# Performance work log

Hardware: AMD Instinct MI355X
Metric: run time of the kernel (lower is better)

Reference implementation:

```python
import jax, jax.numpy as jnp
import numpy as np

N_SRC = 50000   # source nodes in the block
N_DST = 50000   # destination nodes
E = 800000      # edges (avg in-degree 16, every dst has >=1 edge)
D = 256         # hidden_dim
V = 50000       # vocab_size
C = 104         # n_classes (POJ-104)


def setup_inputs() -> dict:
    key = jax.random.key(0)
    k1, k2, k3, k4, k5, k6 = jax.random.split(key, 6)
    token_id = jax.random.randint(k1, (N_SRC,), 0, V, dtype=jnp.int32)
    src_idx = jax.random.randint(k2, (E,), 0, N_SRC, dtype=jnp.int32)
    # every dst node gets at least one in-edge (DGL raises on 0-in-degree),
    # remaining edges land on random dst nodes; sorted so edges are grouped by dst
    extra = jax.random.randint(k3, (E - N_DST,), 0, N_DST, dtype=jnp.int32)
    dst_idx = jnp.sort(jnp.concatenate([jnp.arange(N_DST, dtype=jnp.int32), extra]))
    emb = jax.random.normal(k4, (V, D), dtype=jnp.float32)  # nn.Embedding default N(0,1)
    W = jax.random.normal(k5, (D, D), dtype=jnp.float32) / jnp.sqrt(D)
    b = jnp.zeros((D,), dtype=jnp.float32)
    Wc = jax.random.normal(k6, (C, D), dtype=jnp.float32) / jnp.sqrt(D)
    bc = jnp.zeros((C,), dtype=jnp.float32)
    return {"emb": emb, "W": W, "b": b, "Wc": Wc, "bc": bc,
            "token_id": token_id, "src_idx": src_idx, "dst_idx": dst_idx}


def reference(emb, W, b, Wc, bc, token_id, src_idx, dst_idx):
    # embedding gather for source nodes (first_layer branch)
    feat_src = emb[token_id]                  # [N_SRC, D]
    # message: copy_u -> mailbox messages per edge
    msgs = feat_src[src_idx]                  # [E, D]
    # per-dst segment stats (dst_idx is sorted / grouped by dst)
    deg = jax.ops.segment_sum(jnp.ones((E,), dtype=jnp.int32), dst_idx,
                              num_segments=N_DST)            # [N_DST]
    sum_all = jax.ops.segment_sum(msgs, dst_idx, num_segments=N_DST)  # [N_DST, D]
    # DGL mailbox reducer: last message in the segment is the 'current input',
    # the rest are children summed through CodeRNNCell: x = cur + relu(W @ sum_children + b)
    last_idx = jnp.cumsum(deg) - 1            # index of last edge per dst segment
    last_msg = msgs[last_idx]                 # [N_DST, D]
    child_sum = sum_all - last_msg            # sum of msgs excluding the last one
    rnn_out = last_msg + jax.nn.relu(child_sum @ W.T + b)
    # length == 1 segments bypass the RNN cell entirely: ft = the single message
    ft = jnp.where((deg == 1)[:, None], last_msg, rnn_out)   # [N_DST, D]
    # final classifier
    return ft @ Wc.T + bc                     # [N_DST, C]
```

## Files before the change

kernel.cpp:

```cpp
#include <hip/hip_runtime.h>
#include <hip/hip_bf16.h>

#define DD 256
#define CC 104
#define NSL 8

typedef __bf16 bf16x8 __attribute__((ext_vector_type(8)));
typedef float  f32x4  __attribute__((ext_vector_type(4)));

__device__ inline float bu2f(unsigned short u) {
    return __uint_as_float(((unsigned)u) << 16);
}
__device__ inline unsigned short f2bu(float f) {
    __hip_bfloat16 h = __float2bfloat16(f);
    return *reinterpret_cast<unsigned short*>(&h);
}

__global__ void prep_all(
    const int* __restrict__ token_id,
    const int* __restrict__ src_idx,
    const int* __restrict__ dst_idx,
    int* __restrict__ seg_start,
    int* __restrict__ seg_end,
    int* __restrict__ etp,
    int* __restrict__ last_tok,
    int E, int PB,
    const float* __restrict__ W,
    const float* __restrict__ Wc,
    __hip_bfloat16* __restrict__ Wfrag,
    __hip_bfloat16* __restrict__ Wcfrag)
{
    const int b = blockIdx.x;
    const int t = threadIdx.x;
    if (b < PB) {
        int e = b * 256 + t;
        if (e >= E) return;
        int d = dst_idx[e];
        int tok = token_id[src_idx[e]];
        int lastf = (e == E - 1 || dst_idx[e + 1] != d) ? 1 : 0;
        etp[e] = tok | ((d & 15) << 16) | (lastf << 20);
        if (e == 0 || dst_idx[e - 1] != d) seg_start[d] = e;
        if (lastf) { seg_end[d] = e + 1; last_tok[d] = tok; }
        return;
    }
    if (b < PB + 32) {
        int idx  = (b - PB) * 256 + t;
        int lane = idx & 63, g = idx >> 6;
        int nt = g & 15, k0 = g >> 4;
        int r = nt * 16 + (lane & 15);
        int c = k0 * 32 + (lane >> 4) * 8;
        const float* src = W + (size_t)r * DD + c;
        float4 v0 = *(const float4*)(src);
        float4 v1 = *(const float4*)(src + 4);
        uint4 pk;
        pk.x = (unsigned)f2bu(v0.x) | ((unsigned)f2bu(v0.y) << 16);
        pk.y = (unsigned)f2bu(v0.z) | ((unsigned)f2bu(v0.w) << 16);
        pk.z = (unsigned)f2bu(v1.x) | ((unsigned)f2bu(v1.y) << 16);
        pk.w = (unsigned)f2bu(v1.z) | ((unsigned)f2bu(v1.w) << 16);
        *(uint4*)(Wfrag + (size_t)idx * 8) = pk;
        return;
    }
    {
        int idx  = (b - PB - 32) * 256 + t;
        int lane = idx & 63, g = idx >> 6;
        int nt = g & 7, k0 = g >> 3;
        int r = nt * 16 + (lane & 15);
        int c = k0 * 32 + (lane >> 4) * 8;
        float4 v0 = make_float4(0.f,0.f,0.f,0.f);
        float4 v1 = make_float4(0.f,0.f,0.f,0.f);
        if (r < CC) {
            const float* src = Wc + (size_t)r * DD + c;
            v0 = *(const float4*)(src);
            v1 = *(const float4*)(src + 4);
        }
        uint4 pk;
        pk.x = (unsigned)f2bu(v0.x) | ((unsigned)f2bu(v0.y) << 16);
        pk.y = (unsigned)f2bu(v0.z) | ((unsigned)f2bu(v0.w) << 16);
        pk.z = (unsigned)f2bu(v1.x) | ((unsigned)f2bu(v1.y) << 16);
        pk.w = (unsigned)f2bu(v1.z) | ((unsigned)f2bu(v1.w) << 16);
        *(uint4*)(Wcfrag + (size_t)idx * 8) = pk;
    }
}

__global__ __launch_bounds__(256, 3) void we_gemm(
    const float* __restrict__ emb,
    const __hip_bfloat16* __restrict__ Wfrag,
    __hip_bfloat16* __restrict__ Webuf,
    __hip_bfloat16* __restrict__ embb,
    int V)
{
    __shared__ __hip_bfloat16 lds[32 * 512];
    const int t    = threadIdx.x;
    const int lane = t & 63;
    const int w    = t >> 6;
    const int quad = lane >> 4;
    const int l16  = lane & 15;
    const int mrow = blockIdx.x * 64 + w * 16 + l16;
    const int row  = min(mrow, V - 1);

    bf16x8 bfrag[8];
#pragma unroll
    for (int k0 = 0; k0 < 8; ++k0) {
        const float* src = emb + (size_t)row * DD + k0 * 32 + quad * 8;
        float4 v0 = *(const float4*)(src);
        float4 v1 = *(const float4*)(src + 4);
        uint4 pk;
        pk.x = (unsigned)f2bu(v0.x) | ((unsigned)f2bu(v0.y) << 16);
        pk.y = (unsigned)f2bu(v0.z) | ((unsigned)f2bu(v0.w) << 16);
        pk.z = (unsigned)f2bu(v1.x) | ((unsigned)f2bu(v1.y) << 16);
        pk.w = (unsigned)f2bu(v1.z) | ((unsigned)f2bu(v1.w) << 16);
        bfrag[k0] = *(bf16x8*)&pk;
        if (mrow < V)
            *(uint4*)(embb + (size_t)k0 * V * 32 + (size_t)row * 32 + quad * 8) = pk;
    }

    f32x4 acc[16];
#pragma unroll
    for (int nt = 0; nt < 16; ++nt) acc[nt] = (f32x4){0.f,0.f,0.f,0.f};

    for (int p = 0; p < 4; ++p) {
        if (p) __syncthreads();
#pragma unroll
        for (int it = 0; it < 8; ++it) {
            int idx = it * 256 + t;
            *(uint4*)(lds + (size_t)idx * 8) =
                *(const uint4*)(Wfrag + (size_t)p * 16384 + (size_t)idx * 8);
        }
        __syncthreads();
#pragma unroll
        for (int kl = 0; kl < 2; ++kl) {
            int k0 = p * 2 + kl;
#pragma unroll
            for (int nt = 0; nt < 16; ++nt) {
                bf16x8 wf = *(const bf16x8*)(lds + (kl * 16 + nt) * 512 + lane * 8);
                acc[nt] = __builtin_amdgcn_mfma_f32_16x16x32_bf16(wf, bfrag[k0], acc[nt], 0, 0, 0);
            }
        }
    }

    if (mrow < V) {
#pragma unroll
        for (int nt = 0; nt < 16; ++nt) {
            int c0 = nt * 16 + quad * 4;
            ushort4 o;
            o.x = f2bu(acc[nt][0]);
            o.y = f2bu(acc[nt][1]);
            o.z = f2bu(acc[nt][2]);
            o.w = f2bu(acc[nt][3]);
            *(ushort4*)(Webuf + (size_t)(c0 >> 5) * V * 32 +
                        (size_t)mrow * 32 + (c0 & 31)) = o;
        }
    }
}

__global__ __launch_bounds__(256, 4) void seg_mfma(
    const __hip_bfloat16* __restrict__ Webuf,
    const __hip_bfloat16* __restrict__ embb,
    const int* __restrict__ etp,
    const int* __restrict__ seg_start,
    const int* __restrict__ seg_end,
    const int* __restrict__ last_tok,
    const float* __restrict__ bvec,
    __hip_bfloat16* __restrict__ ftb,
    int n_dst, int V, int E)
{
    __shared__ unsigned char      ldsB[4][2304];
    __shared__ unsigned long long ldsC[4][4];
    const int t   = threadIdx.x;
    const int wv  = t >> 6;
    const int l   = t & 63;
    const int sl  = blockIdx.x & 7;
    const int g   = (blockIdx.x >> 3) * 4 + wv;
    const int d0  = g * 16;
    if (d0 >= n_dst) return;
    const int d1  = min(d0 + 16, n_dst);
    const int S   = seg_start[d0];
    const int End = seg_end[d1 - 1];
    const int l15 = l & 15;
    const int kb  = (l >> 4) * 8;
    const int k   = l >> 1;
    const int half= l & 1;
    const __hip_bfloat16* wsl = Webuf + (size_t)sl * V * 32;
    const __hip_bfloat16* esl = embb  + (size_t)sl * V * 32;
    unsigned char*      myB = ldsB[wv];
    unsigned long long* myC = ldsC[wv];

    f32x4 acc0 = {0.f,0.f,0.f,0.f};
    f32x4 acc1 = {0.f,0.f,0.f,0.f};
    const int R = (End - S + 31) >> 5;

    for (int r = 0; r < R; ++r) {
        int e  = S + 32 * r + k;
        int ec = min(e, End - 1);
        int m  = etp[ec];
        int tok = m & 0xFFFF;
        const __hip_bfloat16* src = wsl + (size_t)tok * 32 + half * 16;
        uint4 Q0 = *(const uint4*)(src);
        uint4 Q1 = *(const uint4*)(src + 8);
        unsigned char* dstB = myB + k * 72 + half * 32;
        *(uint2*)(dstB)      = make_uint2(Q0.x, Q0.y);
        *(uint2*)(dstB + 8)  = make_uint2(Q0.z, Q0.w);
        *(uint2*)(dstB + 16) = make_uint2(Q1.x, Q1.y);
        *(uint2*)(dstB + 24) = make_uint2(Q1.z, Q1.w);
        int code = (e < End && !((m >> 20) & 1)) ? ((m >> 16) & 15) : 255;
        if (half == 0) ((unsigned char*)myC)[k] = (unsigned char)code;
        unsigned long long c8 = myC[l >> 4];
        unsigned mw0, mw1, mw2, mw3;
        {
            unsigned ul15 = (unsigned)l15;
            mw0 = (((unsigned)(c8 >>  0) & 0xFFu) == ul15 ? 0x3F80u : 0u)
                | (((unsigned)(c8 >>  8) & 0xFFu) == ul15 ? 0x3F800000u : 0u);
            mw1 = (((unsigned)(c8 >> 16) & 0xFFu) == ul15 ? 0x3F80u : 0u)
                | (((unsigned)(c8 >> 24) & 0xFFu) == ul15 ? 0x3F800000u : 0u);
            mw2 = (((unsigned)(c8 >> 32) & 0xFFu) == ul15 ? 0x3F80u : 0u)
                | (((unsigned)(c8 >> 40) & 0xFFu) == ul15 ? 0x3F800000u : 0u);
            mw3 = (((unsigned)(c8 >> 48) & 0xFFu) == ul15 ? 0x3F80u : 0u)
                | (((unsigned)(c8 >> 56) & 0xFFu) == ul15 ? 0x3F800000u : 0u);
        }
        uint4 mq = make_uint4(mw0, mw1, mw2, mw3);
        bf16x8 bm = *(bf16x8*)&mq;
#pragma unroll
        for (int h = 0; h < 2; ++h) {
            const unsigned char* ab = myB + h * 32 + l15 * 2;
            unsigned aw0, aw1, aw2, aw3;
            aw0 = (unsigned)*(const unsigned short*)(ab + (kb + 0) * 72)
                | ((unsigned)*(const unsigned short*)(ab + (kb + 1) * 72) << 16);
            aw1 = (unsigned)*(const unsigned short*)(ab + (kb + 2) * 72)
                | ((unsigned)*(const unsigned short*)(ab + (kb + 3) * 72) << 16);
            aw2 = (unsigned)*(const unsigned short*)(ab + (kb + 4) * 72)
                | ((unsigned)*(const unsigned short*)(ab + (kb + 5) * 72) << 16);
            aw3 = (unsigned)*(const unsigned short*)(ab + (kb + 6) * 72)
                | ((unsigned)*(const unsigned short*)(ab + (kb + 7) * 72) << 16);
            uint4 aq = make_uint4(aw0, aw1, aw2, aw3);
            bf16x8 am = *(bf16x8*)&aq;
            if (h == 0) acc0 = __builtin_amdgcn_mfma_f32_16x16x32_bf16(am, bm, acc0, 0, 0, 0);
            else        acc1 = __builtin_amdgcn_mfma_f32_16x16x32_bf16(am, bm, acc1, 0, 0, 0);
        }
    }

    int dst = d0 + l15;
    bool dok = dst < n_dst;
    int dc = min(dst, n_dst - 1);
    int lt  = last_tok[dc];
    int nch = seg_end[dc] - seg_start[dc] - 1;
    bool gate = nch > 0;
    int q = (l >> 4) * 4;
    ushort4 lm0 = *(const ushort4*)(esl + (size_t)lt * 32 + q);
    ushort4 lm1 = *(const ushort4*)(esl + (size_t)lt * 32 + 16 + q);
    float4 b0 = *(const float4*)(bvec + sl * 32 + q);
    float4 b1 = *(const float4*)(bvec + sl * 32 + 16 + q);
    ushort4 o0, o1;
    o0.x = f2bu(bu2f(lm0.x) + (gate ? fmaxf(acc0[0] + b0.x, 0.f) : 0.f));
    o0.y = f2bu(bu2f(lm0.y) + (gate ? fmaxf(acc0[1] + b0.y, 0.f) : 0.f));
    o0.z = f2bu(bu2f(lm0.z) + (gate ? fmaxf(acc0[2] + b0.z, 0.f) : 0.f));
    o0.w = f2bu(bu2f(lm0.w) + (gate ? fmaxf(acc0[3] + b0.w, 0.f) : 0.f));
    o1.x = f2bu(bu2f(lm1.x) + (gate ? fmaxf(acc1[0] + b1.x, 0.f) : 0.f));
    o1.y = f2bu(bu2f(lm1.y) + (gate ? fmaxf(acc1[1] + b1.y, 0.f) : 0.f));
    o1.z = f2bu(bu2f(lm1.z) + (gate ? fmaxf(acc1[2] + b1.z, 0.f) : 0.f));
    o1.w = f2bu(bu2f(lm1.w) + (gate ? fmaxf(acc1[3] + b1.w, 0.f) : 0.f));
    if (dok) {
        __hip_bfloat16* fb = ftb + (size_t)sl * n_dst * 32 + (size_t)dst * 32;
        *(ushort4*)(fb + q)      = o0;
        *(ushort4*)(fb + 16 + q) = o1;
    }
}

__global__ __launch_bounds__(256, 4) void cls_mfma(
    const __hip_bfloat16* __restrict__ ftb,
    const __hip_bfloat16* __restrict__ Wcfrag,
    const float* __restrict__ bc,
    float* __restrict__ out,
    int M)
{
    __shared__ __hip_bfloat16 lds[32 * 512];
    const int t    = threadIdx.x;
    const int lane = t & 63;
    const int w    = t >> 6;
    const int quad = lane >> 4;
    const int l16  = lane & 15;
    const int mw   = blockIdx.x * 64 + w * 16;

    int mrow = min(mw + l16, M - 1);
    bf16x8 ffrag[8];
#pragma unroll
    for (int k0 = 0; k0 < 8; ++k0)
        ffrag[k0] = *(const bf16x8*)(ftb + (size_t)k0 * M * 32 +
                                     (size_t)mrow * 32 + quad * 8);

    f32x4 acc[8];
#pragma unroll
    for (int nt = 0; nt < 8; ++nt) acc[nt] = (f32x4){0.f,0.f,0.f,0.f};

    for (int p = 0; p < 2; ++p) {
        if (p) __syncthreads();
#pragma unroll
        for (int it = 0; it < 8; ++it) {
            int idx = it * 256 + t;
            *(uint4*)(lds + (size_t)idx * 8) =
                *(const uint4*)(Wcfrag + (size_t)p * 16384 + (size_t)idx * 8);
        }
        __syncthreads();
#pragma unroll
        for (int kl = 0; kl < 4; ++kl) {
            int k0 = p * 4 + kl;
#pragma unroll
            for (int nt = 0; nt < 8; ++nt) {
                bf16x8 wf = *(const bf16x8*)(lds + (kl * 8 + nt) * 512 + lane * 8);
                acc[nt] = __builtin_amdgcn_mfma_f32_16x16x32_bf16(wf, ffrag[k0], acc[nt], 0, 0, 0);
            }
        }
    }

    int m = mw + l16;
    if (m < M) {
#pragma unroll
        for (int nt = 0; nt < 8; ++nt) {
            int c0 = nt * 16 + quad * 4;
            if (c0 <= 100) {
                float4 bia = *(const float4*)(bc + c0);
                float4 o;
                o.x = acc[nt][0] + bia.x;
                o.y = acc[nt][1] + bia.y;
                o.z = acc[nt][2] + bia.z;
                o.w = acc[nt][3] + bia.w;
                *(float4*)(out + (size_t)m * CC + c0) = o;
            }
        }
    }
}

extern "C" void kernel_launch(void* const* d_in, const int* in_sizes, int n_in,
                              void* d_out, int out_size, void* d_ws, size_t ws_size,
                              hipStream_t stream)
{
    const float* emb      = (const float*)d_in[0];
    const float* W        = (const float*)d_in[1];
    const float* bvec     = (const float*)d_in[2];
    const float* Wc       = (const float*)d_in[3];
    const float* bc       = (const float*)d_in[4];
    const int*   token_id = (const int*)d_in[5];
    const int*   src_idx  = (const int*)d_in[6];
    const int*   dst_idx  = (const int*)d_in[7];
    float*       out      = (float*)d_out;

    const int E     = in_sizes[6];
    const int Vemb  = in_sizes[0] / DD;
    const int n_dst = out_size / CC;
    (void)n_in; (void)ws_size;

    char* ws = (char*)d_ws;
    size_t off = 0;
    auto alloc = [&](size_t bytes) {
        void* p = ws + off;
        off = (off + bytes + 255) & ~(size_t)255;
        return p;
    };
    int* seg_start = (int*)alloc((size_t)n_dst * sizeof(int));
    int* seg_end   = (int*)alloc((size_t)n_dst * sizeof(int));
    int* last_tok  = (int*)alloc((size_t)n_dst * sizeof(int));
    int* etp       = (int*)alloc((size_t)E * sizeof(int));
    __hip_bfloat16* embb   = (__hip_bfloat16*)alloc((size_t)Vemb * DD * 2);
    __hip_bfloat16* Webuf  = (__hip_bfloat16*)alloc((size_t)Vemb * DD * 2);
    __hip_bfloat16* ftb    = (__hip_bfloat16*)alloc((size_t)n_dst * DD * 2);
    __hip_bfloat16* Wfrag  = (__hip_bfloat16*)alloc((size_t)128 * 512 * 2);
    __hip_bfloat16* Wcfrag = (__hip_bfloat16*)alloc((size_t)64 * 512 * 2);

    const int PB = (E + 255) / 256;
    const int we_blocks  = (Vemb + 63) / 64;
    const int ngroups    = (n_dst + 15) / 16;
    const int seg_blocks = NSL * ((ngroups + 3) / 4);
    const int cls_blocks = (n_dst + 63) / 64;

    prep_all<<<PB + 48, 256, 0, stream>>>(
        token_id, src_idx, dst_idx, seg_start, seg_end, etp, last_tok, E, PB,
        W, Wc, Wfrag, Wcfrag);
    we_gemm<<<we_blocks, 256, 0, stream>>>(
        emb, Wfrag, Webuf, embb, Vemb);
    seg_mfma<<<seg_blocks, 256, 0, stream>>>(
        Webuf, embb, etp, seg_start, seg_end, last_tok, bvec, ftb,
        n_dst, Vemb, E);
    cls_mfma<<<cls_blocks, 256, 0, stream>>>(
        ftb, Wcfrag, bc, out, n_dst);
}
```

Before: 188.0 us.

## Double-buffer LDS gather and use ds_read_b64_tr_b16 transpose loads in seg_mfma

The segment-reduction MFMA loop now prefetches the next round's gathered rows into registers while the current round is computed. LDS is double-buffered, so the next tile is written after the MFMAs. The A-operand assembly, previously sixteen 2-byte LDS reads with shifts and ORs, becomes four ds_read_b64_tr_b16 transposing reads over a new swizzled LDS layout. This targets global-load latency and LDS instruction overhead, at the cost of more registers and inline asm with hard-coded offsets and a full lgkmcnt wait.

```diff
diff --git a/kernel.cpp b/kernel.cpp
--- a/kernel.cpp
+++ b/kernel.cpp
@@ -7,6 +7,7 @@
 
 typedef __bf16 bf16x8 __attribute__((ext_vector_type(8)));
 typedef float  f32x4  __attribute__((ext_vector_type(4)));
+typedef unsigned u32x2 __attribute__((ext_vector_type(2)));
 
 __device__ inline float bu2f(unsigned short u) {
     return __uint_as_float(((unsigned)u) << 16);
@@ -164,8 +165,8 @@
     __hip_bfloat16* __restrict__ ftb,
     int n_dst, int V, int E)
 {
-    __shared__ unsigned char      ldsB[4][2304];
-    __shared__ unsigned long long ldsC[4][4];
+    __shared__ unsigned char      ldsT[4][2][2048];
+    __shared__ unsigned long long ldsC[4][2][4];
     const int t   = threadIdx.x;
     const int wv  = t >> 6;
     const int l   = t & 63;
@@ -177,34 +178,49 @@
     const int S   = seg_start[d0];
     const int End = seg_end[d1 - 1];
     const int l15 = l & 15;
-    const int kb  = (l >> 4) * 8;
     const int k   = l >> 1;
     const int half= l & 1;
+    const int sp   = (k >> 2) & 1;
+    const int srho = ((k >> 3) << 2) | (k & 3);
+    const unsigned woff  = (unsigned)(half * 1024 + sp * 512 + srho * 32);
+    const unsigned troff = (unsigned)(((l >> 4) << 7) + (l15 << 3));
     const __hip_bfloat16* wsl = Webuf + (size_t)sl * V * 32;
     const __hip_bfloat16* esl = embb  + (size_t)sl * V * 32;
-    unsigned char*      myB = ldsB[wv];
-    unsigned long long* myC = ldsC[wv];
 
     f32x4 acc0 = {0.f,0.f,0.f,0.f};
     f32x4 acc1 = {0.f,0.f,0.f,0.f};
     const int R = (End - S + 31) >> 5;
-
-    for (int r = 0; r < R; ++r) {
+    const int rmax = R - 1;
+
+    uint4 Q0, Q1; int code;
+    auto GATHER = [&](int r, uint4& A0, uint4& A1, int& cd) {
         int e  = S + 32 * r + k;
         int ec = min(e, End - 1);
         int m  = etp[ec];
         int tok = m & 0xFFFF;
         const __hip_bfloat16* src = wsl + (size_t)tok * 32 + half * 16;
-        uint4 Q0 = *(const uint4*)(src);
-        uint4 Q1 = *(const uint4*)(src + 8);
-        unsigned char* dstB = myB + k * 72 + half * 32;
-        *(uint2*)(dstB)      = make_uint2(Q0.x, Q0.y);
-        *(uint2*)(dstB + 8)  = make_uint2(Q0.z, Q0.w);
-        *(uint2*)(dstB + 16) = make_uint2(Q1.x, Q1.y);
-        *(uint2*)(dstB + 24) = make_uint2(Q1.z, Q1.w);
-        int code = (e < End && !((m >> 20) & 1)) ? ((m >> 16) & 15) : 255;
-        if (half == 0) ((unsigned char*)myC)[k] = (unsigned char)code;
-        unsigned long long c8 = myC[l >> 4];
+        A0 = *(const uint4*)(src);
+        A1 = *(const uint4*)(src + 8);
+        cd = (e < End && !((m >> 20) & 1)) ? ((m >> 16) & 15) : 255;
+    };
+    auto WRITE = [&](int buf, const uint4& A0, const uint4& A1, int cd) {
+        unsigned char* mb = &ldsT[wv][buf][0];
+        *(uint4*)(mb + woff)      = A0;
+        *(uint4*)(mb + woff + 16) = A1;
+        if (half == 0)
+            ((unsigned char*)&ldsC[wv][buf][0])[k] = (unsigned char)cd;
+    };
+
+    GATHER(0, Q0, Q1, code);
+    WRITE(0, Q0, Q1, code);
+
+    for (int r = 0; r < R; ++r) {
+        int rn = min(r + 1, rmax);
+        GATHER(rn, Q0, Q1, code);
+        __builtin_amdgcn_sched_barrier(0);
+
+        const int buf = r & 1;
+        unsigned long long c8 = ldsC[wv][buf][l >> 4];
         unsigned mw0, mw1, mw2, mw3;
         {
             unsigned ul15 = (unsigned)l15;
@@ -219,23 +235,28 @@
         }
         uint4 mq = make_uint4(mw0, mw1, mw2, mw3);
         bf16x8 bm = *(bf16x8*)&mq;
-#pragma unroll
-        for (int h = 0; h < 2; ++h) {
-            const unsigned char* ab = myB + h * 32 + l15 * 2;
-            unsigned aw0, aw1, aw2, aw3;
-            aw0 = (unsigned)*(const unsigned short*)(ab + (kb + 0) * 72)
-                | ((unsigned)*(const unsigned short*)(ab + (kb + 1) * 72) << 16);
-            aw1 = (unsigned)*(const unsigned short*)(ab + (kb + 2) * 72)
-                | ((unsigned)*(const unsigned short*)(ab + (kb + 3) * 72) << 16);
-            aw2 = (unsigned)*(const unsigned short*)(ab + (kb + 4) * 72)
-                | ((unsigned)*(const unsigned short*)(ab + (kb + 5) * 72) << 16);
-            aw3 = (unsigned)*(const unsigned short*)(ab + (kb + 6) * 72)
-                | ((unsigned)*(const unsigned short*)(ab + (kb + 7) * 72) << 16);
-            uint4 aq = make_uint4(aw0, aw1, aw2, aw3);
-            bf16x8 am = *(bf16x8*)&aq;
-            if (h == 0) acc0 = __builtin_amdgcn_mfma_f32_16x16x32_bf16(am, bm, acc0, 0, 0, 0);
-            else        acc1 = __builtin_amdgcn_mfma_f32_16x16x32_bf16(am, bm, acc1, 0, 0, 0);
-        }
+
+        unsigned base = (unsigned)(uintptr_t)&ldsT[wv][buf][0] + troff;
+        u32x2 r00, r01, r10, r11;
+        asm volatile(
+            "ds_read_b64_tr_b16 %0, %4\n\t"
+            "ds_read_b64_tr_b16 %1, %4 offset:512\n\t"
+            "ds_read_b64_tr_b16 %2, %4 offset:1024\n\t"
+            "ds_read_b64_tr_b16 %3, %4 offset:1536\n\t"
+            "s_waitcnt lgkmcnt(0)"
+            : "=&v"(r00), "=&v"(r01), "=&v"(r10), "=&v"(r11)
+            : "v"(base)
+            : "memory");
+        __builtin_amdgcn_sched_barrier(0);
+
+        uint4 a0q = make_uint4(r00[0], r00[1], r01[0], r01[1]);
+        uint4 a1q = make_uint4(r10[0], r10[1], r11[0], r11[1]);
+        bf16x8 am0 = *(bf16x8*)&a0q;
+        bf16x8 am1 = *(bf16x8*)&a1q;
+        acc0 = __builtin_amdgcn_mfma_f32_16x16x32_bf16(am0, bm, acc0, 0, 0, 0);
+        acc1 = __builtin_amdgcn_mfma_f32_16x16x32_bf16(am1, bm, acc1, 0, 0, 0);
+
+        WRITE((r + 1) & 1, Q0, Q1, code);
     }
 
     int dst = d0 + l15;
```

After: 187.8 us. Within noise of the previous version (-0.1%).
